# Performance work log

Measured on AMD Instinct MI355X. Metric: run time of the kernel, lower is better.

The kernel has to match this reference:

```python
import jax, jax.numpy as jnp
import numpy as np

NV, NC = 4096, 16384        # n_vars, n_clauses
VL, CL = 8, 8               # vlabel_dim (ground_dim), clabel_dim
VE, CE = 128, 128           # vemb_dim, cemb_dim
ITERS = 4                   # max_iters
LN_EPS = 1e-5


def setup_inputs() -> dict:
    key = jax.random.key(0)
    ks = jax.random.split(key, 10)
    return {
        "vlabels": jax.random.normal(ks[0], (NV, VL), jnp.float32),
        "clabels": jax.random.normal(ks[1], (NC, CL), jnp.float32),
        "cmat_pos": jax.random.uniform(ks[2], (NC, NV), jnp.float32),
        "cmat_neg": jax.random.uniform(ks[3], (NC, NV), jnp.float32),
        "W_V_pos": jax.random.normal(ks[4], (VL + VE, CE), jnp.float32),
        "W_V_neg": jax.random.normal(ks[5], (VL + VE, CE), jnp.float32),
        "B_V": jax.random.normal(ks[6], (CE,), jnp.float32),
        "W_C_pos": jax.random.normal(ks[7], (CL + CE, VE), jnp.float32),
        "W_C_neg": jax.random.normal(ks[8], (CL + CE, VE), jnp.float32),
        "B_C": jax.random.normal(ks[9], (VE,), jnp.float32),
        "ln_gamma": jnp.ones((VE,), jnp.float32),
        "ln_beta": jnp.zeros((VE,), jnp.float32),
    }


def _layernorm(x, gamma, beta):
    mu = jnp.mean(x, axis=-1, keepdims=True)
    var = jnp.var(x, axis=-1, keepdims=True)
    return (x - mu) * jax.lax.rsqrt(var + LN_EPS) * gamma + beta


def reference(vlabels, clabels, cmat_pos, cmat_neg,
              W_V_pos, W_V_neg, B_V, W_C_pos, W_C_neg, B_C,
              ln_gamma, ln_beta):
    n_vars = vlabels.shape[0]
    vmat_pos = cmat_pos.T  # [NV, NC]
    vmat_neg = cmat_neg.T
    vembs0 = jnp.zeros((n_vars, VE), vlabels.dtype)

    def step(vembs, _):
        vs = jnp.concatenate([vlabels, vembs], axis=1)          # [NV, VL+VE]
        pv = vs @ W_V_pos                                       # [NV, CE]
        nv = vs @ W_V_neg
        cembs = jax.nn.relu(cmat_pos @ pv + cmat_neg @ nv + B_V)  # [NC, CE]
        cs = jnp.concatenate([clabels, cembs], axis=1)          # [NC, CL+CE]
        pc = cs @ W_C_pos                                       # [NC, VE]
        nc = cs @ W_C_neg
        v = jax.nn.relu(vmat_pos @ pc + vmat_neg @ nc + B_C)    # [NV, VE]
        v = _layernorm(v, ln_gamma, ln_beta)
        return v, None

    vembs, _ = jax.lax.scan(step, vembs0, None, length=ITERS)
    return vembs
```

## Files before the change

kernel.cpp:

```cpp
#include <hip/hip_runtime.h>

#define NVV 4096
#define NCC 16384

typedef __attribute__((ext_vector_type(8))) short short8;
typedef __attribute__((ext_vector_type(4))) float f32x4;

__device__ __forceinline__ short f2bf(float f) {
  union { float f; unsigned u; } v; v.f = f;
  unsigned r = v.u + 0x7fffu + ((v.u >> 16) & 1u);
  return (short)(r >> 16);
}

template<typename AT>
__device__ __forceinline__ short8 load8v(const AT* p) {
  if constexpr (sizeof(AT) == 2) {
    return *(const short8*)p;
  } else {
    const f32x4* q = (const f32x4*)p;
    f32x4 a = q[0], b = q[1];
    short8 o;
#pragma unroll
    for (int j = 0; j < 4; ++j) { o[j] = f2bf(a[j]); o[j + 4] = f2bf(b[j]); }
    return o;
  }
}

__global__ __launch_bounds__(256) void k_conv(const float* __restrict__ src,
                                              short* __restrict__ dst, int n8) {
  int i = blockIdx.x * blockDim.x + threadIdx.x;
  const int stride = gridDim.x * blockDim.x;
  for (; i < n8; i += stride) {
    const f32x4* q = (const f32x4*)(src + (size_t)i * 8);
    f32x4 a = q[0], b = q[1];
    short8 o;
#pragma unroll
    for (int j = 0; j < 4; ++j) { o[j] = f2bf(a[j]); o[j + 4] = f2bf(b[j]); }
    *(short8*)(dst + (size_t)i * 8) = o;
  }
}

template<bool FIRST, int NROW>
__global__ __launch_bounds__(128) void k_mlp(
    const float* __restrict__ labels, const float* __restrict__ embs,
    const float* __restrict__ Wp, const float* __restrict__ Wn,
    short* __restrict__ Tp, short* __restrict__ Tn, int Nrows) {
  const int n = threadIdx.x;
  const int m0 = blockIdx.x * NROW;
  float ap[NROW] = {}, an[NROW] = {};
  const int JMAX = FIRST ? 8 : 136;
  for (int j = 0; j < JMAX; ++j) {
    const float wp = Wp[j * 128 + n], wn = Wn[j * 128 + n];
#pragma unroll
    for (int r = 0; r < NROW; ++r) {
      const float x = (j < 8) ? labels[(size_t)(m0 + r) * 8 + j]
                              : embs[(size_t)(m0 + r) * 128 + (j - 8)];
      ap[r] = fmaf(x, wp, ap[r]);
      an[r] = fmaf(x, wn, an[r]);
    }
  }
#pragma unroll
  for (int r = 0; r < NROW; ++r) {
    Tp[(size_t)n * Nrows + m0 + r] = f2bf(ap[r]);
    Tn[(size_t)n * Nrows + m0 + r] = f2bf(an[r]);
  }
}

template<typename AT, bool TRANSA, int EPI>
__global__ __launch_bounds__(256) void k_gemm(
    const AT* __restrict__ Ap, const AT* __restrict__ An,
    const short* __restrict__ Bp, const short* __restrict__ Bn,
    const float* __restrict__ bias, float* __restrict__ C,
    int M, int lda, int ldb, int Klen) {
  __shared__ __align__(16) short sA[2][32 * 64];
  __shared__ __align__(16) short sB[2][64 * 64];
  const int tid = threadIdx.x;
  const int w = tid >> 6, l = tid & 63, lr = l & 15, lh = l >> 4;
  const int m0 = blockIdx.x * 32, n0 = blockIdx.y * 64;
  const int Koff = blockIdx.z * Klen;
  f32x4 acc0 = {0.f, 0.f, 0.f, 0.f}, acc1 = {0.f, 0.f, 0.f, 0.f};

  for (int step = 0; step < (Klen >> 6); ++step) {
    const int k0 = Koff + (step << 6);
    __syncthreads();
    if (!TRANSA) {
      const int m = tid >> 3, kc = tid & 7;
      const size_t ga = (size_t)(m0 + m) * lda + k0 + (kc << 3);
      const int ad = (m << 6) + ((kc ^ (m & 7)) << 3);
      *(short8*)&sA[0][ad] = load8v(Ap + ga);
      *(short8*)&sA[1][ad] = load8v(An + ga);
    } else {
      const int r = tid >> 2, c8 = (tid & 3) << 3;
      const size_t ga = (size_t)(k0 + r) * lda + m0 + c8;
      short8 vp = load8v(Ap + ga), vn = load8v(An + ga);
#pragma unroll
      for (int j = 0; j < 8; ++j) {
        const int m = c8 + j;
        const int ad = (m << 6) + ((((r >> 3)) ^ (m & 7)) << 3) + (r & 7);
        sA[0][ad] = vp[j];
        sA[1][ad] = vn[j];
      }
    }
#pragma unroll
    for (int i = 0; i < 2; ++i) {
      const int c = (i << 8) + tid;
      const int n = c >> 3, kc = c & 7;
      const size_t gb = (size_t)(n0 + n) * ldb + k0 + (kc << 3);
      const int ad = (n << 6) + ((kc ^ (n & 7)) << 3);
      *(short8*)&sB[0][ad] = *(const short8*)(Bp + gb);
      *(short8*)&sB[1][ad] = *(const short8*)(Bn + gb);
    }
    __syncthreads();
#pragma unroll
    for (int kh = 0; kh < 2; ++kh) {
      const int kc = (kh << 2) + lh;
      const int bn_ = (w << 4) + lr;
      short8 bp = *(short8*)&sB[0][(bn_ << 6) + ((kc ^ (bn_ & 7)) << 3)];
      short8 bnv = *(short8*)&sB[1][(bn_ << 6) + ((kc ^ (bn_ & 7)) << 3)];
      short8 a0p = *(short8*)&sA[0][(lr << 6) + ((kc ^ (lr & 7)) << 3)];
      short8 a0n = *(short8*)&sA[1][(lr << 6) + ((kc ^ (lr & 7)) << 3)];
      const int m1 = 16 + lr;
      short8 a1p = *(short8*)&sA[0][(m1 << 6) + ((kc ^ (m1 & 7)) << 3)];
      short8 a1n = *(short8*)&sA[1][(m1 << 6) + ((kc ^ (m1 & 7)) << 3)];
      acc0 = __builtin_amdgcn_mfma_f32_16x16x32_bf16(a0p, bp, acc0, 0, 0, 0);
      acc0 = __builtin_amdgcn_mfma_f32_16x16x32_bf16(a0n, bnv, acc0, 0, 0, 0);
      acc1 = __builtin_amdgcn_mfma_f32_16x16x32_bf16(a1p, bp, acc1, 0, 0, 0);
      acc1 = __builtin_amdgcn_mfma_f32_16x16x32_bf16(a1n, bnv, acc1, 0, 0, 0);
    }
  }
  const int n = n0 + (w << 4) + lr;
#pragma unroll
  for (int mf = 0; mf < 2; ++mf) {
    f32x4 a = mf ? acc1 : acc0;
#pragma unroll
    for (int r = 0; r < 4; ++r) {
      const int m = m0 + (mf << 4) + (lh << 2) + r;
      float c = a[r];
      if (EPI == 0) {
        c += bias[n];
        c = fmaxf(c, 0.f);
        C[(size_t)m * 128 + n] = c;
      } else {
        C[((size_t)blockIdx.z * M + m) * 128 + n] = c;
      }
    }
  }
}

__global__ __launch_bounds__(256) void k_reduce_ln(
    const float* __restrict__ part, const float* __restrict__ bias,
    const float* __restrict__ gamma, const float* __restrict__ beta,
    float* __restrict__ out) {
  const int w = threadIdx.x >> 6, l = threadIdx.x & 63;
  const int m = blockIdx.x * 4 + w;
  const int n0 = l << 1;
  float x0 = bias[n0], x1 = bias[n0 + 1];
#pragma unroll
  for (int ks = 0; ks < 4; ++ks) {
    const size_t o = ((size_t)ks * NVV + m) * 128 + n0;
    x0 += part[o];
    x1 += part[o + 1];
  }
  x0 = fmaxf(x0, 0.f);
  x1 = fmaxf(x1, 0.f);
  float s = x0 + x1, q = x0 * x0 + x1 * x1;
#pragma unroll
  for (int off = 32; off; off >>= 1) {
    s += __shfl_xor(s, off);
    q += __shfl_xor(q, off);
  }
  const float mu = s * (1.f / 128.f);
  const float var = q * (1.f / 128.f) - mu * mu;
  const float inv = 1.f / sqrtf(var + 1e-5f);
  out[(size_t)m * 128 + n0]     = (x0 - mu) * inv * gamma[n0] + beta[n0];
  out[(size_t)m * 128 + n0 + 1] = (x1 - mu) * inv * gamma[n0 + 1] + beta[n0 + 1];
}

extern "C" void kernel_launch(void* const* d_in, const int* in_sizes, int n_in,
                              void* d_out, int out_size, void* d_ws, size_t ws_size,
                              hipStream_t stream) {
  const float* vlabels  = (const float*)d_in[0];
  const float* clabels  = (const float*)d_in[1];
  const float* cmat_pos = (const float*)d_in[2];
  const float* cmat_neg = (const float*)d_in[3];
  const float* Wvp = (const float*)d_in[4];
  const float* Wvn = (const float*)d_in[5];
  const float* Bv  = (const float*)d_in[6];
  const float* Wcp = (const float*)d_in[7];
  const float* Wcn = (const float*)d_in[8];
  const float* Bc  = (const float*)d_in[9];
  const float* gam = (const float*)d_in[10];
  const float* bet = (const float*)d_in[11];
  float* out = (float*)d_out;

  char* base = (char*)d_ws;
  size_t off = 0;
  auto carve = [&](size_t b) -> void* {
    void* p = base + off;
    off += (b + 255) & ~(size_t)255;
    return p;
  };
  short* pvT  = (short*)carve((size_t)128 * NVV * 2);
  short* nvT  = (short*)carve((size_t)128 * NVV * 2);
  short* pcT  = (short*)carve((size_t)128 * NCC * 2);
  short* ncT  = (short*)carve((size_t)128 * NCC * 2);
  float* cemb = (float*)carve((size_t)NCC * 128 * 4);
  float* part = (float*)carve((size_t)4 * NVV * 128 * 4);
  short* cmPb = (short*)carve((size_t)NCC * NVV * 2);
  short* cmNb = (short*)carve((size_t)NCC * NVV * 2);
  const bool big = ws_size >= off;

  if (big) {
    k_conv<<<4096, 256, 0, stream>>>(cmat_pos, cmPb, NCC * NVV / 8);
    k_conv<<<4096, 256, 0, stream>>>(cmat_neg, cmNb, NCC * NVV / 8);
  }

  for (int it = 0; it < 4; ++it) {
    if (it == 0)
      k_mlp<true, 16><<<NVV / 16, 128, 0, stream>>>(vlabels, nullptr, Wvp, Wvn, pvT, nvT, NVV);
    else
      k_mlp<false, 16><<<NVV / 16, 128, 0, stream>>>(vlabels, out, Wvp, Wvn, pvT, nvT, NVV);

    if (big)
      k_gemm<short, false, 0><<<dim3(NCC / 32, 2, 1), 256, 0, stream>>>(
          cmPb, cmNb, pvT, nvT, Bv, cemb, NCC, NVV, NVV, NVV);
    else
      k_gemm<float, false, 0><<<dim3(NCC / 32, 2, 1), 256, 0, stream>>>(
          cmat_pos, cmat_neg, pvT, nvT, Bv, cemb, NCC, NVV, NVV, NVV);

    k_mlp<false, 16><<<NCC / 16, 128, 0, stream>>>(clabels, cemb, Wcp, Wcn, pcT, ncT, NCC);

    if (big)
      k_gemm<short, true, 1><<<dim3(NVV / 32, 2, 4), 256, 0, stream>>>(
          cmPb, cmNb, pcT, ncT, nullptr, part, NVV, NVV, NCC, NVV);
    else
      k_gemm<float, true, 1><<<dim3(NVV / 32, 2, 4), 256, 0, stream>>>(
          cmat_pos, cmat_neg, pcT, ncT, nullptr, part, NVV, NVV, NCC, NVV);

    k_reduce_ln<<<NVV / 4, 256, 0, stream>>>(part, Bc, gam, bet, out);
  }
}
```

Before: 1.617 ms.

## Add transposed bf16 copy and direct-to-LDS pipelined MFMA GEMM

The conversion kernel now writes both a row-major and a transposed bf16 copy of each clause matrix through an LDS tile transpose. A new GEMM kernel streams A tiles straight into swizzled LDS with global_load_lds using a 4-deep buffer ring, and prefetches B fragments into registers one step ahead. It interleaves the pos and neg matrices along K, and the transposed GEMM now reads the pre-transposed copy instead of doing a strided transposed access. The MLP kernels drop to 4 rows per block with vectorized stores. This costs an extra 256MB of workspace and more conversion traffic up front.

```diff
diff --git a/kernel.cpp b/kernel.cpp
--- a/kernel.cpp
+++ b/kernel.cpp
@@ -4,6 +4,7 @@
 #define NCC 16384
 
 typedef __attribute__((ext_vector_type(8))) short short8;
+typedef __attribute__((ext_vector_type(4))) short short4v;
 typedef __attribute__((ext_vector_type(4))) float f32x4;
 
 __device__ __forceinline__ short f2bf(float f) {
@@ -38,6 +39,25 @@
     for (int j = 0; j < 4; ++j) { o[j] = f2bf(a[j]); o[j + 4] = f2bf(b[j]); }
     *(short8*)(dst + (size_t)i * 8) = o;
   }
+}
+
+__global__ __launch_bounds__(256) void k_convT(const float* __restrict__ src,
+                                               short* __restrict__ dstN,
+                                               short* __restrict__ dstT,
+                                               int R, int C) {
+  __shared__ short t[32][36];
+  const int r0 = blockIdx.y * 32, c0 = blockIdx.x * 32;
+  const int tr = threadIdx.x >> 3, tc4 = (threadIdx.x & 7) << 2;
+  const f32x4 v = *(const f32x4*)(src + (size_t)(r0 + tr) * C + c0 + tc4);
+  short4v o;
+#pragma unroll
+  for (int j = 0; j < 4; ++j) { o[j] = f2bf(v[j]); t[tc4 + j][tr] = o[j]; }
+  *(short4v*)(dstN + (size_t)(r0 + tr) * C + c0 + tc4) = o;
+  __syncthreads();
+  short4v ot;
+#pragma unroll
+  for (int j = 0; j < 4; ++j) ot[j] = t[tr][tc4 + j];
+  *(short4v*)(dstT + (size_t)(c0 + tr) * R + r0 + tc4) = ot;
 }
 
 template<bool FIRST, int NROW>
@@ -59,10 +79,87 @@
       an[r] = fmaf(x, wn, an[r]);
     }
   }
-#pragma unroll
-  for (int r = 0; r < NROW; ++r) {
-    Tp[(size_t)n * Nrows + m0 + r] = f2bf(ap[r]);
-    Tn[(size_t)n * Nrows + m0 + r] = f2bf(an[r]);
+  short4v vp, vn;
+#pragma unroll
+  for (int r = 0; r < NROW; ++r) { vp[r] = f2bf(ap[r]); vn[r] = f2bf(an[r]); }
+  *(short4v*)(Tp + (size_t)n * Nrows + m0) = vp;
+  *(short4v*)(Tn + (size_t)n * Nrows + m0) = vn;
+}
+
+template<int EPI>
+__global__ __launch_bounds__(256) void k_gemm_f(
+    const short* __restrict__ Ap, const short* __restrict__ An,
+    const short* __restrict__ Bp, const short* __restrict__ Bn,
+    const float* __restrict__ bias, float* __restrict__ C,
+    int M, int lda, int ldb, int Klen) {
+  __shared__ __align__(16) short sA[4][2048];
+  const int tid = threadIdx.x;
+  const int w = tid >> 6, l = tid & 63, lr = l & 15, lh = l >> 4;
+  const int m0 = blockIdx.x * 32, n0 = blockIdx.y * 64;
+  const int Koff = (int)blockIdx.z * Klen;
+  const int T = (Klen >> 6) << 1;
+  f32x4 acc0 = {0.f, 0.f, 0.f, 0.f}, acc1 = {0.f, 0.f, 0.f, 0.f};
+
+  const int sm = tid >> 3;
+  const int skc = (tid & 7) ^ (sm & 7);
+  const size_t aRowOff = (size_t)(m0 + sm) * lda + Koff + (skc << 3);
+  const size_t bRowOff = (size_t)(n0 + (w << 4) + lr) * ldb + Koff + (lh << 3);
+
+  auto stageA = [&](int t, int buf) {
+    const short* A = (t & 1) ? An : Ap;
+    const short* g = A + aRowOff + ((t >> 1) << 6);
+    __builtin_amdgcn_global_load_lds(
+        (const __attribute__((address_space(1))) void*)g,
+        (__attribute__((address_space(3))) void*)(&sA[buf][w << 9]),
+        16, 0, 0);
+  };
+  auto loadB = [&](int t, short8& b0, short8& b1) {
+    const short* B = (t & 1) ? Bn : Bp;
+    const short* g = B + bRowOff + ((t >> 1) << 6);
+    b0 = *(const short8*)g;
+    b1 = *(const short8*)(g + 32);
+  };
+
+  stageA(0, 0);
+  short8 bC0, bC1, bN0, bN1;
+  loadB(0, bC0, bC1);
+  stageA(1, 1);
+
+  for (int t = 0; t < T; ++t) {
+    const int t1 = (t + 1 < T) ? t + 1 : t + 1 - T;
+    const int t2 = (t + 2 < T) ? t + 2 : t + 2 - T;
+    loadB(t1, bN0, bN1);
+    stageA(t2, (t + 2) & 3);
+    asm volatile("s_waitcnt vmcnt(6)" ::: "memory");
+    __builtin_amdgcn_s_barrier();
+    asm volatile("" ::: "memory");
+    const int buf = t & 3;
+    const int kc0 = lh, kc1 = 4 + lh;
+    const int ma = lr, mb = 16 + lr;
+    short8 a00 = *(const short8*)&sA[buf][(ma << 6) + ((kc0 ^ (ma & 7)) << 3)];
+    short8 a01 = *(const short8*)&sA[buf][(mb << 6) + ((kc0 ^ (mb & 7)) << 3)];
+    short8 a10 = *(const short8*)&sA[buf][(ma << 6) + ((kc1 ^ (ma & 7)) << 3)];
+    short8 a11 = *(const short8*)&sA[buf][(mb << 6) + ((kc1 ^ (mb & 7)) << 3)];
+    acc0 = __builtin_amdgcn_mfma_f32_16x16x32_bf16(a00, bC0, acc0, 0, 0, 0);
+    acc1 = __builtin_amdgcn_mfma_f32_16x16x32_bf16(a01, bC0, acc1, 0, 0, 0);
+    acc0 = __builtin_amdgcn_mfma_f32_16x16x32_bf16(a10, bC1, acc0, 0, 0, 0);
+    acc1 = __builtin_amdgcn_mfma_f32_16x16x32_bf16(a11, bC1, acc1, 0, 0, 0);
+    bC0 = bN0; bC1 = bN1;
+  }
+
+  const int cn = n0 + (w << 4) + lr;
+#pragma unroll
+  for (int mf = 0; mf < 2; ++mf) {
+    f32x4 a = mf ? acc1 : acc0;
+#pragma unroll
+    for (int r = 0; r < 4; ++r) {
+      const int m = m0 + (mf << 4) + (lh << 2) + r;
+      if (EPI == 0) {
+        C[(size_t)m * 128 + cn] = fmaxf(a[r] + bias[cn], 0.f);
+      } else {
+        C[((size_t)blockIdx.z * M + m) * 128 + cn] = a[r];
+      }
+    }
   }
 }
 
@@ -208,29 +305,40 @@
   float* part = (float*)carve((size_t)4 * NVV * 128 * 4);
   short* cmPb = (short*)carve((size_t)NCC * NVV * 2);
   short* cmNb = (short*)carve((size_t)NCC * NVV * 2);
-  const bool big = ws_size >= off;
-
-  if (big) {
+  const size_t needN = off;
+  short* cmTP = (short*)carve((size_t)NCC * NVV * 2);
+  short* cmTN = (short*)carve((size_t)NCC * NVV * 2);
+  const size_t needT = off;
+  const bool big  = ws_size >= needN;
+  const bool bigT = ws_size >= needT;
+
+  if (bigT) {
+    k_convT<<<dim3(NVV / 32, NCC / 32), 256, 0, stream>>>(cmat_pos, cmPb, cmTP, NCC, NVV);
+    k_convT<<<dim3(NVV / 32, NCC / 32), 256, 0, stream>>>(cmat_neg, cmNb, cmTN, NCC, NVV);
+  } else if (big) {
     k_conv<<<4096, 256, 0, stream>>>(cmat_pos, cmPb, NCC * NVV / 8);
     k_conv<<<4096, 256, 0, stream>>>(cmat_neg, cmNb, NCC * NVV / 8);
   }
 
   for (int it = 0; it < 4; ++it) {
     if (it == 0)
-      k_mlp<true, 16><<<NVV / 16, 128, 0, stream>>>(vlabels, nullptr, Wvp, Wvn, pvT, nvT, NVV);
+      k_mlp<true, 4><<<NVV / 4, 128, 0, stream>>>(vlabels, nullptr, Wvp, Wvn, pvT, nvT, NVV);
     else
-      k_mlp<false, 16><<<NVV / 16, 128, 0, stream>>>(vlabels, out, Wvp, Wvn, pvT, nvT, NVV);
+      k_mlp<false, 4><<<NVV / 4, 128, 0, stream>>>(vlabels, out, Wvp, Wvn, pvT, nvT, NVV);
 
     if (big)
-      k_gemm<short, false, 0><<<dim3(NCC / 32, 2, 1), 256, 0, stream>>>(
+      k_gemm_f<0><<<dim3(NCC / 32, 2, 1), 256, 0, stream>>>(
           cmPb, cmNb, pvT, nvT, Bv, cemb, NCC, NVV, NVV, NVV);
     else
       k_gemm<float, false, 0><<<dim3(NCC / 32, 2, 1), 256, 0, stream>>>(
           cmat_pos, cmat_neg, pvT, nvT, Bv, cemb, NCC, NVV, NVV, NVV);
 
-    k_mlp<false, 16><<<NCC / 16, 128, 0, stream>>>(clabels, cemb, Wcp, Wcn, pcT, ncT, NCC);
-
-    if (big)
+    k_mlp<false, 4><<<NCC / 4, 128, 0, stream>>>(clabels, cemb, Wcp, Wcn, pcT, ncT, NCC);
+
+    if (bigT)
+      k_gemm_f<1><<<dim3(NVV / 32, 2, 4), 256, 0, stream>>>(
+          cmTP, cmTN, pcT, ncT, nullptr, part, NVV, NCC, NCC, NCC / 4);
+    else if (big)
       k_gemm<short, true, 1><<<dim3(NVV / 32, 2, 4), 256, 0, stream>>>(
           cmPb, cmNb, pcT, ncT, nullptr, part, NVV, NVV, NCC, NVV);
     else
```

Result: slower. 1.681 ms (+3.9%).

## Add 128x128 MFMA GEMM with direct-to-LDS loads and pre-transposed bf16 clause matrices

Applied to the files above, without the earlier changes.

Adds a new GEMM kernel with 128x128 tiles per block, XOR-swizzled LDS and global_load_lds async copies, so the two bf16 matrix products get more data reuse than the old 32x64 tiles. The clause matrices are converted to bf16 in both normal and transposed form, so the variable-side GEMM reads a row-major operand instead of a transposed one. Both GEMMs use split-K partial sums, and the clause-side bias, ReLU and split-K reduction are folded into the clause MLP kernel. This needs a much larger workspace (two extra transposed copies) and keeps the old path as a fallback when the workspace is too small.

```diff
diff --git a/kernel.cpp b/kernel.cpp
--- a/kernel.cpp
+++ b/kernel.cpp
@@ -4,6 +4,7 @@
 #define NCC 16384
 
 typedef __attribute__((ext_vector_type(8))) short short8;
+typedef __attribute__((ext_vector_type(4))) short short4v;
 typedef __attribute__((ext_vector_type(4))) float f32x4;
 
 __device__ __forceinline__ short f2bf(float f) {
@@ -40,30 +41,151 @@
   }
 }
 
-template<bool FIRST, int NROW>
+__global__ __launch_bounds__(256) void k_convT(const float* __restrict__ src,
+                                               short* __restrict__ dstN,
+                                               short* __restrict__ dstT,
+                                               int R, int C) {
+  __shared__ short t[32][36];
+  const int r0 = blockIdx.y * 32, c0 = blockIdx.x * 32;
+  const int tr = threadIdx.x >> 3, tc4 = (threadIdx.x & 7) << 2;
+  const f32x4 v = *(const f32x4*)(src + (size_t)(r0 + tr) * C + c0 + tc4);
+  short4v o;
+#pragma unroll
+  for (int j = 0; j < 4; ++j) { o[j] = f2bf(v[j]); t[tc4 + j][tr] = o[j]; }
+  *(short4v*)(dstN + (size_t)(r0 + tr) * C + c0 + tc4) = o;
+  __syncthreads();
+  short4v ot;
+#pragma unroll
+  for (int j = 0; j < 4; ++j) ot[j] = t[tr][tc4 + j];
+  *(short4v*)(dstT + (size_t)(c0 + tr) * R + r0 + tc4) = ot;
+}
+
+template<int SRC, int NROW>
 __global__ __launch_bounds__(128) void k_mlp(
     const float* __restrict__ labels, const float* __restrict__ embs,
+    const float* __restrict__ bias,
     const float* __restrict__ Wp, const float* __restrict__ Wn,
-    short* __restrict__ Tp, short* __restrict__ Tn, int Nrows) {
+    short* __restrict__ Tp, short* __restrict__ Tn, int Nrows, int KS) {
+  __shared__ float xs[NROW][130];
   const int n = threadIdx.x;
   const int m0 = blockIdx.x * NROW;
+  if (SRC == 2) {
+#pragma unroll
+    for (int r = 0; r < NROW; ++r) {
+      const size_t m = m0 + r;
+      float v = bias[n];
+      for (int ks = 0; ks < KS; ++ks)
+        v += embs[((size_t)ks * NCC + m) * 128 + n];
+      xs[r][n] = fmaxf(v, 0.f);
+    }
+    __syncthreads();
+  }
   float ap[NROW] = {}, an[NROW] = {};
-  const int JMAX = FIRST ? 8 : 136;
+  const int JMAX = (SRC == 0) ? 8 : 136;
   for (int j = 0; j < JMAX; ++j) {
     const float wp = Wp[j * 128 + n], wn = Wn[j * 128 + n];
 #pragma unroll
     for (int r = 0; r < NROW; ++r) {
-      const float x = (j < 8) ? labels[(size_t)(m0 + r) * 8 + j]
-                              : embs[(size_t)(m0 + r) * 128 + (j - 8)];
+      float x;
+      if (j < 8)            x = labels[(size_t)(m0 + r) * 8 + j];
+      else if (SRC == 2)    x = xs[r][j - 8];
+      else                  x = embs[(size_t)(m0 + r) * 128 + (j - 8)];
       ap[r] = fmaf(x, wp, ap[r]);
       an[r] = fmaf(x, wn, an[r]);
     }
   }
-#pragma unroll
-  for (int r = 0; r < NROW; ++r) {
-    Tp[(size_t)n * Nrows + m0 + r] = f2bf(ap[r]);
-    Tn[(size_t)n * Nrows + m0 + r] = f2bf(an[r]);
-  }
+  short8 vp0, vn0, vp1, vn1;
+#pragma unroll
+  for (int r = 0; r < 8; ++r) {
+    vp0[r] = f2bf(ap[r]); vn0[r] = f2bf(an[r]);
+    vp1[r] = f2bf(ap[8 + r]); vn1[r] = f2bf(an[8 + r]);
+  }
+  *(short8*)(Tp + (size_t)n * Nrows + m0) = vp0;
+  *(short8*)(Tp + (size_t)n * Nrows + m0 + 8) = vp1;
+  *(short8*)(Tn + (size_t)n * Nrows + m0) = vn0;
+  *(short8*)(Tn + (size_t)n * Nrows + m0 + 8) = vn1;
+}
+
+__global__ __launch_bounds__(256, 2) void k_gemm4(
+    const short* __restrict__ Ap, const short* __restrict__ An,
+    const short* __restrict__ Bp, const short* __restrict__ Bn,
+    float* __restrict__ C, int M, int lda, int ldb, int Klen) {
+  __shared__ __align__(16) short sA[2][8192];
+  __shared__ __align__(16) short sB[2][8192];
+  const int tid = threadIdx.x;
+  const int w = tid >> 6, l = tid & 63, lr = l & 15, lh = l >> 4;
+  const int wr = w >> 1, wc = w & 1;
+  const int m0 = blockIdx.x * 128;
+  const int Koff = (int)blockIdx.z * Klen;
+  const int T = Klen >> 6;
+
+  const int srow = tid >> 3;
+  const int scol = ((tid & 7) ^ (srow & 7)) << 3;
+  const short* gA0 = Ap + (size_t)(m0 + srow) * lda + Koff + scol;
+  const short* gA1 = An + (size_t)(m0 + srow) * lda + Koff + scol;
+  const short* gB0 = Bp + (size_t)srow * ldb + Koff + scol;
+  const short* gB1 = Bn + (size_t)srow * ldb + Koff + scol;
+
+  f32x4 acc[4][4] = {};
+
+  for (int step = 0; step < T; ++step) {
+    const int k0 = step << 6;
+#pragma unroll
+    for (int i = 0; i < 4; ++i) {
+      const size_t ra = (size_t)(i * 32) * lda + k0;
+      const size_t rb = (size_t)(i * 32) * ldb + k0;
+      const int ld = i * 2048 + w * 512;
+      __builtin_amdgcn_global_load_lds(
+          (const __attribute__((address_space(1))) void*)(gA0 + ra),
+          (__attribute__((address_space(3))) void*)(&sA[0][ld]), 16, 0, 0);
+      __builtin_amdgcn_global_load_lds(
+          (const __attribute__((address_space(1))) void*)(gA1 + ra),
+          (__attribute__((address_space(3))) void*)(&sA[1][ld]), 16, 0, 0);
+      __builtin_amdgcn_global_load_lds(
+          (const __attribute__((address_space(1))) void*)(gB0 + rb),
+          (__attribute__((address_space(3))) void*)(&sB[0][ld]), 16, 0, 0);
+      __builtin_amdgcn_global_load_lds(
+          (const __attribute__((address_space(1))) void*)(gB1 + rb),
+          (__attribute__((address_space(3))) void*)(&sB[1][ld]), 16, 0, 0);
+    }
+    __syncthreads();
+#pragma unroll
+    for (int kk = 0; kk < 2; ++kk) {
+#pragma unroll
+      for (int mat = 0; mat < 2; ++mat) {
+        const int kc = (kk << 2) + lh;
+        short8 a[4], b[4];
+#pragma unroll
+        for (int mi = 0; mi < 4; ++mi) {
+          const int row = (wr << 6) + (mi << 4) + lr;
+          a[mi] = *(const short8*)&sA[mat][(row << 6) + ((kc ^ (row & 7)) << 3)];
+        }
+#pragma unroll
+        for (int nj = 0; nj < 4; ++nj) {
+          const int n = (wc << 6) + (nj << 4) + lr;
+          b[nj] = *(const short8*)&sB[mat][(n << 6) + ((kc ^ (n & 7)) << 3)];
+        }
+#pragma unroll
+        for (int mi = 0; mi < 4; ++mi)
+#pragma unroll
+          for (int nj = 0; nj < 4; ++nj)
+            acc[mi][nj] = __builtin_amdgcn_mfma_f32_16x16x32_bf16(
+                a[mi], b[nj], acc[mi][nj], 0, 0, 0);
+      }
+    }
+    __syncthreads();
+  }
+
+  const size_t crow0 = (size_t)blockIdx.z * M + m0 + (wr << 6) + (lh << 2);
+#pragma unroll
+  for (int mi = 0; mi < 4; ++mi)
+#pragma unroll
+    for (int nj = 0; nj < 4; ++nj) {
+      const int col = (wc << 6) + (nj << 4) + lr;
+#pragma unroll
+      for (int r = 0; r < 4; ++r)
+        C[(crow0 + (mi << 4) + r) * 128 + col] = acc[mi][nj][r];
+    }
 }
 
 template<typename AT, bool TRANSA, int EPI>
@@ -147,6 +269,7 @@
   }
 }
 
+template<int KS>
 __global__ __launch_bounds__(256) void k_reduce_ln(
     const float* __restrict__ part, const float* __restrict__ bias,
     const float* __restrict__ gamma, const float* __restrict__ beta,
@@ -156,7 +279,7 @@
   const int n0 = l << 1;
   float x0 = bias[n0], x1 = bias[n0 + 1];
 #pragma unroll
-  for (int ks = 0; ks < 4; ++ks) {
+  for (int ks = 0; ks < KS; ++ks) {
     const size_t o = ((size_t)ks * NVV + m) * 128 + n0;
     x0 += part[o];
     x1 += part[o + 1];
@@ -194,21 +317,65 @@
   float* out = (float*)d_out;
 
   char* base = (char*)d_ws;
-  size_t off = 0;
-  auto carve = [&](size_t b) -> void* {
-    void* p = base + off;
-    off += (b + 255) & ~(size_t)255;
-    return p;
-  };
-  short* pvT  = (short*)carve((size_t)128 * NVV * 2);
-  short* nvT  = (short*)carve((size_t)128 * NVV * 2);
-  short* pcT  = (short*)carve((size_t)128 * NCC * 2);
-  short* ncT  = (short*)carve((size_t)128 * NCC * 2);
-  float* cemb = (float*)carve((size_t)NCC * 128 * 4);
-  float* part = (float*)carve((size_t)4 * NVV * 128 * 4);
-  short* cmPb = (short*)carve((size_t)NCC * NVV * 2);
-  short* cmNb = (short*)carve((size_t)NCC * NVV * 2);
-  const bool big = ws_size >= off;
+  const size_t SZ_vT  = (size_t)128 * NVV * 2;
+  const size_t SZ_cT  = (size_t)128 * NCC * 2;
+  const size_t SZ_cm  = (size_t)NCC * NVV * 2;
+  const size_t SZ_p8  = (size_t)NCC * 128 * 4;
+
+  size_t o = 0;
+  auto al = [&](size_t b) { size_t p = o; o += (b + 255) & ~(size_t)255; return p; };
+  short* pvT  = (short*)(base + al(SZ_vT));
+  short* nvT  = (short*)(base + al(SZ_vT));
+  short* pcT  = (short*)(base + al(SZ_cT));
+  short* ncT  = (short*)(base + al(SZ_cT));
+  short* cmPb = (short*)(base + al(SZ_cm));
+  short* cmNb = (short*)(base + al(SZ_cm));
+  short* cmTP = (short*)(base + al(SZ_cm));
+  short* cmTN = (short*)(base + al(SZ_cm));
+  float* part = (float*)(base + al(4 * SZ_p8));
+  const size_t needFA = o;
+  const size_t needFB = needFA - 2 * SZ_p8;
+
+  const bool fastA = ws_size >= needFA;
+  const bool fastB = !fastA && ws_size >= needFB;
+
+  if (fastA || fastB) {
+    const int SK1 = fastA ? 4 : 2;
+    const int SK2 = fastA ? 16 : 8;
+    k_convT<<<dim3(NVV / 32, NCC / 32), 256, 0, stream>>>(cmat_pos, cmPb, cmTP, NCC, NVV);
+    k_convT<<<dim3(NVV / 32, NCC / 32), 256, 0, stream>>>(cmat_neg, cmNb, cmTN, NCC, NVV);
+
+    for (int it = 0; it < 4; ++it) {
+      if (it == 0)
+        k_mlp<0, 16><<<NVV / 16, 128, 0, stream>>>(vlabels, nullptr, nullptr, Wvp, Wvn, pvT, nvT, NVV, 0);
+      else
+        k_mlp<1, 16><<<NVV / 16, 128, 0, stream>>>(vlabels, out, nullptr, Wvp, Wvn, pvT, nvT, NVV, 0);
+
+      k_gemm4<<<dim3(NCC / 128, 1, SK1), 256, 0, stream>>>(
+          cmPb, cmNb, pvT, nvT, part, NCC, NVV, NVV, NVV / SK1);
+      k_mlp<2, 16><<<NCC / 16, 128, 0, stream>>>(clabels, part, Bv, Wcp, Wcn, pcT, ncT, NCC, SK1);
+
+      k_gemm4<<<dim3(NVV / 128, 1, SK2), 256, 0, stream>>>(
+          cmTP, cmTN, pcT, ncT, part, NVV, NCC, NCC, NCC / SK2);
+      if (fastA)
+        k_reduce_ln<16><<<NVV / 4, 256, 0, stream>>>(part, Bc, gam, bet, out);
+      else
+        k_reduce_ln<8><<<NVV / 4, 256, 0, stream>>>(part, Bc, gam, bet, out);
+    }
+    return;
+  }
+
+  o = 0;
+  pvT  = (short*)(base + al(SZ_vT));
+  nvT  = (short*)(base + al(SZ_vT));
+  pcT  = (short*)(base + al(SZ_cT));
+  ncT  = (short*)(base + al(SZ_cT));
+  part = (float*)(base + al(2 * SZ_p8));
+  float* cemb = (float*)(base + al(SZ_p8));
+  cmPb = (short*)(base + al(SZ_cm));
+  cmNb = (short*)(base + al(SZ_cm));
+  const size_t needN = o;
+  const bool big = ws_size >= needN;
 
   if (big) {
     k_conv<<<4096, 256, 0, stream>>>(cmat_pos, cmPb, NCC * NVV / 8);
@@ -217,26 +384,24 @@
 
   for (int it = 0; it < 4; ++it) {
     if (it == 0)
-      k_mlp<true, 16><<<NVV / 16, 128, 0, stream>>>(vlabels, nullptr, Wvp, Wvn, pvT, nvT, NVV);
+      k_mlp<0, 16><<<NVV / 16, 128, 0, stream>>>(vlabels, nullptr, nullptr, Wvp, Wvn, pvT, nvT, NVV, 0);
     else
-      k_mlp<false, 16><<<NVV / 16, 128, 0, stream>>>(vlabels, out, Wvp, Wvn, pvT, nvT, NVV);
-
-    if (big)
-      k_gemm<short, false, 0><<<dim3(NCC / 32, 2, 1), 256, 0, stream>>>(
-          cmPb, cmNb, pvT, nvT, Bv, cemb, NCC, NVV, NVV, NVV);
-    else
+      k_mlp<1, 16><<<NVV / 16, 128, 0, stream>>>(vlabels, out, nullptr, Wvp, Wvn, pvT, nvT, NVV, 0);
+
+    if (big) {
+      k_gemm4<<<dim3(NCC / 128, 1, 2), 256, 0, stream>>>(
+          cmPb, cmNb, pvT, nvT, part, NCC, NVV, NVV, NVV / 2);
+      k_mlp<2, 16><<<NCC / 16, 128, 0, stream>>>(clabels, part, Bv, Wcp, Wcn, pcT, ncT, NCC, 2);
+      k_gemm<short, true, 1><<<dim3(NVV / 32, 2, 4), 256, 0, stream>>>(
+          cmPb, cmNb, pcT, ncT, nullptr, part, NVV, NVV, NCC, NVV);
+      k_reduce_ln<4><<<NVV / 4, 256, 0, stream>>>(part, Bc, gam, bet, out);
+    } else {
       k_gemm<float, false, 0><<<dim3(NCC / 32, 2, 1), 256, 0, stream>>>(
           cmat_pos, cmat_neg, pvT, nvT, Bv, cemb, NCC, NVV, NVV, NVV);
-
-    k_mlp<false, 16><<<NCC / 16, 128, 0, stream>>>(clabels, cemb, Wcp, Wcn, pcT, ncT, NCC);
-
-    if (big)
-      k_gemm<short, true, 1><<<dim3(NVV / 32, 2, 4), 256, 0, stream>>>(
-          cmPb, cmNb, pcT, ncT, nullptr, part, NVV, NVV, NCC, NVV);
-    else
+      k_mlp<1, 16><<<NCC / 16, 128, 0, stream>>>(clabels, cemb, nullptr, Wcp, Wcn, pcT, ncT, NCC, 0);
       k_gemm<float, true, 1><<<dim3(NVV / 32, 2, 4), 256, 0, stream>>>(
           cmat_pos, cmat_neg, pcT, ncT, nullptr, part, NVV, NVV, NCC, NVV);
-
-    k_reduce_ln<<<NVV / 4, 256, 0, stream>>>(part, Bc, gam, bet, out);
-  }
-}
+      k_reduce_ln<4><<<NVV / 4, 256, 0, stream>>>(part, Bc, gam, bet, out);
+    }
+  }
+}
```

Result: faster. 1.455 ms (-10.0%).
